# Performance work log

Hardware: AMD Instinct MI355X
Metric: run time of the kernel (lower is better)

## Reference

```python
import jax, jax.numpy as jnp
import numpy as np
import math

B, L, D, P, H, WIN, MAXLEN = 2, 2048, 256, 32, 4, 5, 16384


def setup_inputs() -> dict:
    key = jax.random.key(0)
    ks = iter(jax.random.split(key, 40))
    def w(shape, scale=0.05):
        return jax.random.normal(next(ks), shape, jnp.float32) * scale
    inp = {
        'x': jax.random.normal(next(ks), (B, L, D), jnp.float32),
        'pos_phases': jax.random.normal(next(ks), (MAXLEN, P), jnp.float32) * math.pi,
        # mem1_content_encoder
        'w_content': w((D, D)), 'b_content': jnp.zeros((D,), jnp.float32),
        # head_offset_predictors (stacked over H): Linear(D+P, D//2) -> GELU -> Linear(D//2, P+1)
        'hop_w1': w((H, D // 2, D + P)), 'hop_b1': jnp.zeros((H, D // 2), jnp.float32),
        'hop_w2': w((H, P + 1, D // 2)), 'hop_b2': jnp.zeros((H, P + 1), jnp.float32),
        # content_phase_encoder
        'w_cpe': w((P, D)), 'b_cpe': jnp.zeros((P,), jnp.float32),
        # value_encoder
        'w_val': w((D, D)), 'b_val': jnp.zeros((D,), jnp.float32),
        # kv_context_encoder
        'w_ctx': w((D, D)), 'b_ctx': jnp.zeros((D,), jnp.float32),
        # kv_storage_key: Linear(2D, D) -> GELU -> Linear(D, P)
        'kv_w1': w((D, 2 * D)), 'kv_b1': jnp.zeros((D,), jnp.float32),
        'kv_w2': w((P, D)), 'kv_b2': jnp.zeros((P,), jnp.float32),
        # store_gate: Linear(D, D//2) -> GELU -> Linear(D//2, 1) -> Sigmoid
        'sg_w1': w((D // 2, D)), 'sg_b1': jnp.zeros((D // 2,), jnp.float32),
        'sg_w2': w((1, D // 2)), 'sg_b2': jnp.zeros((1,), jnp.float32),
        # to_out: LayerNorm(D) -> Linear(D, D)
        'ln_g': jnp.ones((D,), jnp.float32), 'ln_b': jnp.zeros((D,), jnp.float32),
        'w_out': w((D, D)), 'b_out': jnp.zeros((D,), jnp.float32),
    }
    return inp


def reference(x, pos_phases, w_content, b_content, hop_w1, hop_b1, hop_w2, hop_b2,
              w_cpe, b_cpe, w_val, b_val, w_ctx, b_ctx, kv_w1, kv_b1, kv_w2, kv_b2,
              sg_w1, sg_b1, sg_w2, sg_b2, ln_g, ln_b, w_out, b_out):
    gelu = lambda t: jax.nn.gelu(t, approximate=False)  # torch exact GELU
    pp = pos_phases[:L]                      # (L,P)
    pos_cos, pos_sin = jnp.cos(pp), jnp.sin(pp)

    # ---- phasor memory 1: position-bound content cumsum ----
    content = x @ w_content.T + b_content    # (B,L,D)
    mem1_cos = jnp.cumsum(pos_cos[None, :, :, None] * content[:, :, None, :], axis=1)  # (B,L,P,D)
    mem1_sin = jnp.cumsum(pos_sin[None, :, :, None] * content[:, :, None, :], axis=1)

    # ---- per-head learned offsets ----
    offset_input = jnp.concatenate([x, jnp.broadcast_to(pp[None], (B, L, P))], axis=-1)  # (B,L,D+P)
    h1 = gelu(jnp.einsum('blf,hgf->bhlg', offset_input, hop_w1) + hop_b1[None, :, None, :])
    off = jnp.einsum('bhlg,hpg->bhlp', h1, hop_w2) + hop_b2[None, :, None, :]  # (B,H,L,P+1)
    center = jnp.tanh(off[..., :P]) * math.pi    # (B,H,L,P)
    ww = jax.nn.sigmoid(off[..., P:]) * 2 + 0.1  # (B,H,L,1)

    head_ret = jnp.zeros((B, H, L, D), x.dtype)
    tot_w = jnp.zeros((B, H, L, 1), x.dtype)
    half = WIN // 2
    for delta in range(-half, half + 1):
        wgt = jnp.exp(-0.5 * delta ** 2 / (ww ** 2 + 1e-6))
        op = center + delta * 0.1
        oc, os = jnp.cos(op), jnp.sin(op)
        qc = pos_cos[None, None] * oc - pos_sin[None, None] * os
        qs = pos_sin[None, None] * oc + pos_cos[None, None] * os
        ret = (jnp.einsum('blpd,bhlp->bhld', mem1_cos, qc)
               + jnp.einsum('blpd,bhlp->bhld', mem1_sin, qs)) / math.sqrt(P)
        head_ret = head_ret + wgt * ret
        tot_w = tot_w + wgt
    multi_head_out = (head_ret / (tot_w + 1e-6)).mean(axis=1)  # (B,L,D)

    # ---- kv phasor memory ----
    key_ph = jnp.tanh(x @ w_cpe.T + b_cpe) * math.pi            # (B,L,P)
    values = x @ w_val.T + b_val                                 # (B,L,D)
    store_gate = jax.nn.sigmoid(gelu(x @ sg_w1.T + sg_b1) @ sg_w2.T + sg_b2)  # (B,L,1)
    ctx = x @ w_ctx.T + b_ctx
    ctx_avg = jnp.cumsum(ctx, axis=1) / jnp.arange(1, L + 1, dtype=x.dtype)[None, :, None]
    storage_in = jnp.concatenate([x, ctx_avg], axis=-1)          # (B,L,2D)
    sp = jnp.tanh(gelu(storage_in @ kv_w1.T + kv_b1) @ kv_w2.T + kv_b2) * math.pi  # (B,L,P)
    gated_v = values * store_gate                                # (B,L,D)
    kv_cos = jnp.cumsum(jnp.cos(sp)[..., None] * gated_v[:, :, None, :], axis=1)  # (B,L,P,D)
    kv_sin = jnp.cumsum(jnp.sin(sp)[..., None] * gated_v[:, :, None, :], axis=1)
    gate_cum = jnp.clip(jnp.cumsum(store_gate, axis=1), 1.0, None)  # (B,L,1)
    kv_ret = (jnp.einsum('blpd,blp->bld', kv_cos, jnp.cos(key_ph))
              + jnp.einsum('blpd,blp->bld', kv_sin, jnp.sin(key_ph)))
    kv_ret = kv_ret / (jnp.sqrt(gate_cum) * math.sqrt(P))

    # ---- output projection ----
    combined = multi_head_out + kv_ret
    mu = combined.mean(-1, keepdims=True)
    var = combined.var(-1, keepdims=True)
    ln = (combined - mu) / jnp.sqrt(var + 1e-5) * ln_g + ln_b
    return x + ln @ w_out.T + b_out
```

## Files before the change

kernel.cpp:

```cpp
#include <hip/hip_runtime.h>
#include <hip/hip_bf16.h>

#define BB 2
#define LL 2048
#define DD 256
#define PP 32
#define PX 64
#define NROW (BB*LL)
#define COLS 1440
#define KIN 288
#define CC 64
#define NC (LL/CC)
#define PI_F 3.14159265358979323846f

typedef __attribute__((ext_vector_type(8))) short bf16x8;
typedef __attribute__((ext_vector_type(4))) float f32x4;

__device__ __forceinline__ float gelu_f(float v){
    return 0.5f*v*(1.0f+erff(v*0.70710678118654752440f));
}
__device__ __forceinline__ float sigm_f(float v){
    return 1.0f/(1.0f+expf(-v));
}
__device__ __forceinline__ short f2b(float v){
    __hip_bfloat16 h = __float2bfloat16(v);
    return *reinterpret_cast<short*>(&h);
}
__device__ __forceinline__ float b2f(unsigned short u){
    unsigned int x = ((unsigned int)u)<<16;
    return __uint_as_float(x);
}

__global__ void kprep(const float* w_content,const float* w_val,const float* w_ctx,
                      const float* w_cpe,const float* sg_w1,const float* hop_w1,
                      const float* b_content,const float* b_val,const float* b_ctx,
                      const float* b_cpe,const float* sg_b1,const float* hop_b1,
                      const float* pos_phases,const float* kv_w1,const float* kv_w2,
                      const float* hop_w2,const float* x,
                      short* W_catb,float* bias_cat,float* w2mem,
                      short* kvw1b,short* kvw2b,float* hop_w2T,
                      short* Xb,short* Xin2b){
    int idx = blockIdx.x*256 + threadIdx.x;
    int n1 = COLS*KIN;
    if (idx < n1){
        int row = idx / KIN, k = idx % KIN;
        float v = 0.f;
        if      (row < 256){ if (k<256) v = w_content[row*256+k]; }
        else if (row < 512){ if (k<256) v = w_val[(row-256)*256+k]; }
        else if (row < 768){ if (k<256) v = w_ctx[(row-512)*256+k]; }
        else if (row < 800){ if (k<256) v = w_cpe[(row-768)*256+k]; }
        else if (row < 928){ if (k<256) v = sg_w1[(row-800)*256+k]; }
        else               { v = hop_w1[(row-928)*288 + k]; }
        W_catb[idx] = f2b(v);
        return;
    }
    idx -= n1;
    if (idx < COLS){
        int row = idx; float v = 0.f;
        if      (row < 256) v = b_content[row];
        else if (row < 512) v = b_val[row-256];
        else if (row < 768) v = b_ctx[row-512];
        else if (row < 800) v = b_cpe[row-768];
        else if (row < 928) v = sg_b1[row-800];
        else                v = hop_b1[row-928];
        bias_cat[row] = v;
        return;
    }
    idx -= COLS;
    if (idx < LL*PP){
        int l = idx/PP, p = idx%PP;
        float ph = pos_phases[l*PP+p];
        w2mem[l*PX+p]     = cosf(ph);
        w2mem[l*PX+32+p]  = sinf(ph);
        return;
    }
    idx -= LL*PP;
    if (idx < 256*512){ kvw1b[idx] = f2b(kv_w1[idx]); return; }
    idx -= 256*512;
    if (idx < 32*256){ kvw2b[idx] = f2b(kv_w2[idx]); return; }
    idx -= 32*256;
    if (idx < 128*132){
        int k=idx/132, o=idx%132;
        hop_w2T[idx] = hop_w2[o*128+k];
        return;
    }
    idx -= 128*132;
    if (idx < NROW*KIN){
        int r = idx / KIN, d = idx % KIN;
        float v;
        if (d < 256){ v = x[(size_t)r*DD + d]; Xin2b[(size_t)r*512 + d] = f2b(v); }
        else          v = pos_phases[(r % LL)*PP + (d-256)];
        Xb[idx] = f2b(v);
    }
}

__global__ __launch_bounds__(256) void kA_gemm(const short* Xb,const short* Wb,short* Yb){
    int t=threadIdx.x;
    int wid=t>>6, l=t&63;
    int q=blockIdx.x;
    int ct=q%15, rt=q/15;
    int r0=rt*64 + wid*16;
    int c0=ct*96;
    int lr=l&15, lk=(l>>4)*8;
    const short* ap = Xb + (size_t)(r0+lr)*KIN + lk;
    const short* bp = Wb + (size_t)(c0+lr)*KIN + lk;
    f32x4 acc[6];
    #pragma unroll
    for (int f=0;f<6;f++) acc[f]=(f32x4){0.f,0.f,0.f,0.f};
    for (int ks=0;ks<9;ks++){
        bf16x8 a = *(const bf16x8*)(ap + ks*32);
        #pragma unroll
        for (int f=0;f<6;f++){
            bf16x8 b = *(const bf16x8*)(bp + (size_t)f*16*KIN + ks*32);
            acc[f] = __builtin_amdgcn_mfma_f32_16x16x32_bf16(a,b,acc[f],0,0,0);
        }
    }
    int orow = r0 + (l>>4)*4;
    int ocol = c0 + lr;
    #pragma unroll
    for (int f=0;f<6;f++){
        #pragma unroll
        for (int qq=0;qq<4;qq++){
            Yb[(size_t)(orow+qq)*COLS + ocol + 16*f] = f2b(acc[f][qq]);
        }
    }
}

__global__ __launch_bounds__(256,4) void kA_post(const short* Yb,const float* bias_cat,
        const float* sg_w2,const float* sg_b2,
        const float* hop_w2T,const float* hop_b2,const float* pos_phases,
        short* contentb,short* gatedvb,float* ctx,float* key_ph,
        float* store_gate,float* coef_mem){
    __shared__ float yb[4][1448];
    __shared__ float red[4][32];
    __shared__ float offb[4][136];
    __shared__ float scl[4][4];
    __shared__ float sgvv[4];
    int t=threadIdx.x;
    int r0=blockIdx.x*4;
    {
        const ushort4* Yu4 = (const ushort4*)(Yb) + (size_t)r0*360;
        #pragma unroll
        for (int i=0;i<6;i++){
            int chunk=i*256+t;
            if (chunk<1440){
                int r=chunk/360, c=(chunk%360)*4;
                ushort4 s4 = Yu4[chunk];
                float4 bc = *(const float4*)&bias_cat[c];
                yb[r][c+0]=b2f(s4.x)+bc.x;
                yb[r][c+1]=b2f(s4.y)+bc.y;
                yb[r][c+2]=b2f(s4.z)+bc.z;
                yb[r][c+3]=b2f(s4.w)+bc.w;
            }
        }
    }
    __syncthreads();
    #pragma unroll
    for (int r=0;r<4;r++){
        contentb[(size_t)(r0+r)*DD+t] = f2b(yb[r][t]);
        ctx[(size_t)(r0+r)*DD+t]      = yb[r][512+t];
    }
    #pragma unroll
    for (int j=0;j<8;j++){
        int idx=j*256+t, r=idx>>9, g=idx&511;
        yb[r][928+g] = gelu_f(yb[r][928+g]);
    }
    if (t<128){
        int r=t>>5, j=t&31;
        float s=0.f;
        #pragma unroll
        for (int k=0;k<4;k++){
            int jj=j+32*k;
            s += gelu_f(yb[r][800+jj])*sg_w2[jj];
        }
        red[r][j]=s;
        key_ph[(size_t)(r0+r)*PP+j] = tanhf(yb[r][768+j])*PI_F;
    }
    __syncthreads();
    if (t<128){
        int r=t>>5;
        float s=red[r][t&31];
        #pragma unroll
        for (int off=16;off>=1;off>>=1) s += __shfl_down(s,off,32);
        if ((t&31)==0){
            float g=sigm_f(s+sg_b2[0]);
            sgvv[r]=g;
            store_gate[r0+r]=g;
        }
    }
    for (int sIdx=t; sIdx<528; sIdx+=256){
        int r=sIdx/132, o=sIdx%132, h=o/33;
        const float* yh=&yb[r][928+h*128];
        float a0=0.f,a1=0.f,a2=0.f,a3=0.f;
        #pragma unroll 8
        for (int k=0;k<128;k+=4){
            a0 += hop_w2T[(size_t)(k+0)*132+o]*yh[k+0];
            a1 += hop_w2T[(size_t)(k+1)*132+o]*yh[k+1];
            a2 += hop_w2T[(size_t)(k+2)*132+o]*yh[k+2];
            a3 += hop_w2T[(size_t)(k+3)*132+o]*yh[k+3];
        }
        offb[r][o]=a0+a1+a2+a3+hop_b2[o];
    }
    __syncthreads();
    #pragma unroll
    for (int r=0;r<4;r++) gatedvb[(size_t)(r0+r)*DD+t]=f2b(yb[r][256+t]*sgvv[r]);
    if (t<16){
        int r=t>>2, h=t&3;
        const float c01=0.99500416527802576610f;
        const float c02=0.98006657784124163112f;
        float ww=sigm_f(offb[r][h*33+32])*2.0f+0.1f;
        float iw=1.0f/(ww*ww+1e-6f);
        float w1=expf(-0.5f*iw);
        float w2=expf(-2.0f*iw);
        float tot=1.0f+2.0f*w1+2.0f*w2;
        float Wc =1.0f+2.0f*w1*c01+2.0f*w2*c02;
        scl[r][h]=Wc/((tot+1e-6f)*5.65685424949238019520f*4.0f);
    }
    __syncthreads();
    if (t<128){
        int r=t>>5, p=t&31;
        int l=(r0+r)%LL;
        float ppv=pos_phases[l*PP+p];
        float ca=0.f, sb=0.f;
        #pragma unroll
        for (int h=0;h<4;h++){
            float center=tanhf(offb[r][h*33+p])*PI_F;
            float ang=ppv+center;
            float sc=scl[r][h];
            ca+=sc*cosf(ang);
            sb+=sc*sinf(ang);
        }
        coef_mem[(size_t)(r0+r)*PX+p]=ca;
        coef_mem[(size_t)(r0+r)*PX+32+p]=sb;
    }
}

__global__ void k3a_ctxsum(const float* ctx,float* ctxcs){
    int t=threadIdx.x;
    int bi=blockIdx.x;
    int c=bi%NC, b=bi/NC;
    float s=0.f;
    for (int i=0;i<CC;i++) s += ctx[((size_t)b*LL + c*CC + i)*DD + t];
    ctxcs[(size_t)(b*NC+c)*DD + t] = s;
}
__global__ void k3c_ctxavg(const float* ctx,const float* ctxcs,short* Xin2b){
    int t=threadIdx.x;
    int bi=blockIdx.x;
    int c=bi%NC, b=bi/NC;
    float run=0.f;
    for (int cc=0;cc<c;cc++) run += ctxcs[(size_t)(b*NC+cc)*DD+t];
    for (int i=0;i<CC;i++){
        int l = c*CC+i;
        run += ctx[((size_t)b*LL+l)*DD + t];
        Xin2b[((size_t)b*LL+l)*512 + 256 + t] = f2b(run/(float)(l+1));
    }
}

__global__ __launch_bounds__(256) void kgate(const float* store_gate,const float* key_ph,
                                             float* coefkv){
    __shared__ float sh[2048];
    __shared__ float red[256];
    __shared__ float rsgS[64];
    int t=threadIdx.x, q=blockIdx.x;
    int c=q&31, b=q>>5;
    int n=(c+1)*CC;
    for (int i=t;i<n;i+=256) sh[i]=store_gate[(size_t)b*LL+i];
    __syncthreads();
    float p=0.f;
    for (int i=t;i<c*CC;i+=256) p+=sh[i];
    red[t]=p;
    __syncthreads();
    for (int off=128;off>=1;off>>=1){
        if (t<off) red[t]+=red[t+off];
        __syncthreads();
    }
    float S0=red[0];
    if (t<64){
        float s=sh[c*CC+t];
        #pragma unroll
        for (int off=1;off<64;off<<=1){
            float v=__shfl_up(s,off);
            if (t>=off) s+=v;
        }
        rsgS[t]=rsqrtf(fmaxf(S0+s,1.0f)*32.0f);
    }
    __syncthreads();
    #pragma unroll
    for (int j=0;j<8;j++){
        int g2=t+j*256;
        int l=g2>>5, pp=g2&31;
        float a=key_ph[((size_t)b*LL + c*CC + l)*PP + pp];
        float rv=rsgS[l];
        coefkv[((size_t)b*LL + c*CC + l)*PX + pp]      = cosf(a)*rv;
        coefkv[((size_t)b*LL + c*CC + l)*PX + 32 + pp] = sinf(a)*rv;
    }
}

__global__ __launch_bounds__(256) void k3d1(const short* Xin2b,const short* kvw1b,
        const float* kv_b1, short* Hb){
    int t=threadIdx.x;
    int wid=t>>6, l=t&63;
    int q=blockIdx.x;
    int nt=q&3, mt=q>>2;
    int r0=mt*64 + wid*16;
    int c0=nt*64;
    int lr=l&15, lk=(l>>4)*8;
    const short* ap = Xin2b + (size_t)(r0+lr)*512 + lk;
    const short* bp = kvw1b + (size_t)(c0+lr)*512 + lk;
    f32x4 acc[4];
    #pragma unroll
    for (int f=0;f<4;f++) acc[f]=(f32x4){0.f,0.f,0.f,0.f};
    for (int ks=0;ks<16;ks++){
        bf16x8 a = *(const bf16x8*)(ap + ks*32);
        #pragma unroll
        for (int f=0;f<4;f++){
            bf16x8 b = *(const bf16x8*)(bp + (size_t)f*16*512 + ks*32);
            acc[f] = __builtin_amdgcn_mfma_f32_16x16x32_bf16(a,b,acc[f],0,0,0);
        }
    }
    int orow = r0 + (l>>4)*4;
    #pragma unroll
    for (int f=0;f<4;f++){
        int oc = c0 + lr + 16*f;
        float bias = kv_b1[oc];
        #pragma unroll
        for (int qq=0;qq<4;qq++){
            Hb[(size_t)(orow+qq)*256 + oc] = f2b(gelu_f(acc[f][qq]+bias));
        }
    }
}

__global__ __launch_bounds__(256) void k3d2(const short* Hb,const short* kvw2b,
        const float* kv_b2, float* w2kv){
    int t=threadIdx.x;
    int wid=t>>6, l=t&63;
    int mt=blockIdx.x;
    int r0=mt*64 + wid*16;
    int lr=l&15, lk=(l>>4)*8;
    const short* ap = Hb + (size_t)(r0+lr)*256 + lk;
    const short* bp = kvw2b + (size_t)lr*256 + lk;
    f32x4 acc0=(f32x4){0.f,0.f,0.f,0.f};
    f32x4 acc1=(f32x4){0.f,0.f,0.f,0.f};
    for (int ks=0;ks<8;ks++){
        bf16x8 a  = *(const bf16x8*)(ap + ks*32);
        bf16x8 b0 = *(const bf16x8*)(bp + ks*32);
        bf16x8 b1 = *(const bf16x8*)(bp + (size_t)16*256 + ks*32);
        acc0 = __builtin_amdgcn_mfma_f32_16x16x32_bf16(a,b0,acc0,0,0,0);
        acc1 = __builtin_amdgcn_mfma_f32_16x16x32_bf16(a,b1,acc1,0,0,0);
    }
    int orow=r0+(l>>4)*4;
    #pragma unroll
    for (int f=0;f<2;f++){
        int p = lr + 16*f;
        float bias = kv_b2[p];
        f32x4 av = f? acc1:acc0;
        #pragma unroll
        for (int qq=0;qq<4;qq++){
            float sp=tanhf(av[qq]+bias)*PI_F;
            w2kv[(size_t)(orow+qq)*PX + p]    = cosf(sp);
            w2kv[(size_t)(orow+qq)*PX + 32+p] = sinf(sp);
        }
    }
}

__global__ __launch_bounds__(256) void k4_chunksum(
        const short* valA,const float* w2A,int w2bA,
        const short* valB,const float* w2B,int w2bB,
        float* CS){
    __shared__ float w2s[CC][PX];
    int t=threadIdx.x, q=blockIdx.x;
    int dq=q&3, c=(q>>2)&31, b=(q>>7)&1, inst=q>>8;
    const short* val = inst? valB:valA;
    const float* w2  = inst? w2B:w2A;
    int w2b          = inst? w2bB:w2bA;
    for (int i=0;i<16;i++){
        int idx=i*256+t;
        int l=idx>>6, p=idx&63;
        w2s[l][p]=w2[(size_t)w2b*b + (size_t)(c*CC+l)*PX + p];
    }
    __syncthreads();
    int d=t&63, pg=t>>6;
    float acc[16];
    #pragma unroll
    for (int j=0;j<16;j++) acc[j]=0.f;
    const short* vp = val + ((size_t)b*LL + c*CC)*DD + dq*64 + d;
    for (int l=0;l<CC;l++){
        float v = b2f((unsigned short)vp[(size_t)l*DD]);
        const float4* wr=(const float4*)&w2s[l][pg*16];
        #pragma unroll
        for (int k=0;k<4;k++){
            float4 w=wr[k];
            acc[4*k]   += w.x*v;
            acc[4*k+1] += w.y*v;
            acc[4*k+2] += w.z*v;
            acc[4*k+3] += w.w*v;
        }
    }
    float* cp = CS + (((size_t)(inst*BB+b)*NC + c)*PX + pg*16)*DD + dq*64 + d;
    #pragma unroll
    for (int j=0;j<16;j++) cp[(size_t)j*DD]=acc[j];
}

__global__ void k5_prefix(float* CS){
    int g=blockIdx.x*256+threadIdx.x;
    int d=g&255, p2=(g>>8)&63, b=(g>>14)&1, inst=g>>15;
    float run=0.f;
    for (int c=0;c<NC;c++){
        size_t idx=(((size_t)(inst*BB+b)*NC+c)*PX+p2)*DD+d;
        float tmp=CS[idx]; CS[idx]=run; run+=tmp;
    }
}

__global__ __launch_bounds__(256) void k6_attn(
        const float* coefA,const float* w2A,int w2bA,const short* valA,float* outA,
        const float* coefB,const float* w2B,int w2bB,const short* valB,float* outB,
        const float* CS){
    __shared__ float coefs[16][PX];
    __shared__ float w2s[CC][PX];
    __shared__ float S[16][CC];
    int t=threadIdx.x, q=blockIdx.x;
    int rq=q&3, qc=(q>>2)&31, b=(q>>7)&1, inst=q>>8;
    const float* coef = inst? coefB:coefA;
    const float* w2   = inst? w2B:w2A;
    int w2b           = inst? w2bB:w2bA;
    const short* val  = inst? valB:valA;
    float* out        = inst? outB:outA;
    int gr0 = rq*16;
    #pragma unroll
    for (int i=0;i<4;i++){
        int idx=i*256+t;
        int r=idx>>6, p=idx&63;
        coefs[r][p]=coef[((size_t)b*LL + qc*CC + gr0 + r)*PX + p];
    }
    for (int i=0;i<16;i++){
        int idx=i*256+t;
        int l=idx>>6, p=idx&63;
        w2s[l][p]=w2[(size_t)w2b*b + (size_t)(qc*CC+l)*PX + p];
    }
    __syncthreads();
    {
        int lp=t&63, rr=t>>6;
        #pragma unroll
        for (int rj=0;rj<4;rj++){
            int r=rr*4+rj;
            int gr=gr0+r;
            float s=0.f;
            if (lp<=gr){
                const float4* cr=(const float4*)&coefs[r][0];
                const float4* wr=(const float4*)&w2s[lp][0];
                #pragma unroll
                for (int k=0;k<16;k++){
                    float4 cv=cr[k], wv=wr[k];
                    s += cv.x*wv.x+cv.y*wv.y+cv.z*wv.z+cv.w*wv.w;
                }
            }
            S[r][lp]=s;
        }
    }
    __syncthreads();
    {
        float acc[16];
        #pragma unroll
        for (int i=0;i<16;i++) acc[i]=0.f;
        const float* pfx = CS + (((size_t)(inst*BB+b)*NC + qc)*PX)*DD + t;
        for (int p=0;p<PX;p++){
            float pf = pfx[(size_t)p*DD];
            #pragma unroll
            for (int i=0;i<16;i++) acc[i] += coefs[i][p]*pf;
        }
        const short* vptr = val + ((size_t)b*LL + qc*CC)*DD + t;
        int kmax = gr0+16;
        for (int lp=0; lp<kmax; lp++){
            float v = b2f((unsigned short)vptr[(size_t)lp*DD]);
            #pragma unroll
            for (int i=0;i<16;i++) acc[i] += S[i][lp]*v;
        }
        float* op = out + ((size_t)b*LL + qc*CC + gr0)*DD + t;
        #pragma unroll
        for (int i=0;i<16;i++) op[(size_t)i*DD] = acc[i];
    }
}

__global__ __launch_bounds__(256) void k7_final(const float* comb,const float* kvout,
        const float* x,const float* ln_g,const float* ln_b,const float* w_out,const float* b_out,
        float* out){
    __shared__ float cb[8][DD];
    __shared__ float red[8][64];
    __shared__ float mvm[8][2];
    int t=threadIdx.x, r0=blockIdx.x*8;
    for (int r=0;r<8;r++){
        float v = comb[(size_t)(r0+r)*DD + t] + kvout[(size_t)(r0+r)*DD + t];
        cb[r][t]=v;
    }
    __syncthreads();
    {
        int rr=t>>5, ii=t&31;
        float s=0.f, s2=0.f;
        #pragma unroll
        for (int j=0;j<8;j++){
            float v=cb[rr][ii*8+j];
            s+=v; s2+=v*v;
        }
        red[rr][ii]=s; red[rr][32+ii]=s2;
    }
    __syncthreads();
    if (t<8){
        float s=0.f,s2=0.f;
        for (int i=0;i<32;i++){ s+=red[t][i]; s2+=red[t][32+i]; }
        float mu=s/256.f;
        float var=s2/256.f - mu*mu;
        mvm[t][0]=mu; mvm[t][1]=rsqrtf(var+1e-5f);
    }
    __syncthreads();
    for (int r=0;r<8;r++){
        float v=(cb[r][t]-mvm[r][0])*mvm[r][1]*ln_g[t]+ln_b[t];
        cb[r][t]=v;
    }
    __syncthreads();
    {
        int c=t;
        const float4* wp=(const float4*)(w_out + (size_t)c*DD);
        float acc[8];
        #pragma unroll
        for (int r=0;r<8;r++) acc[r]=0.f;
        for (int k4=0;k4<64;k4++){
            float4 w=wp[k4];
            #pragma unroll
            for (int r=0;r<8;r++){
                float4 lv=*(const float4*)&cb[r][k4*4];
                acc[r]+=w.x*lv.x+w.y*lv.y+w.z*lv.z+w.w*lv.w;
            }
        }
        #pragma unroll
        for (int r=0;r<8;r++){
            float o = x[(size_t)(r0+r)*DD + c] + acc[r] + b_out[c];
            out[(size_t)(r0+r)*DD + c] = o;
        }
    }
}

extern "C" void kernel_launch(void* const* d_in, const int* in_sizes, int n_in,
                              void* d_out, int out_size, void* d_ws, size_t ws_size,
                              hipStream_t stream){
    (void)in_sizes; (void)n_in; (void)out_size; (void)ws_size;
    const float* x         =(const float*)d_in[0];
    const float* pos_phases=(const float*)d_in[1];
    const float* w_content =(const float*)d_in[2];
    const float* b_content =(const float*)d_in[3];
    const float* hop_w1    =(const float*)d_in[4];
    const float* hop_b1    =(const float*)d_in[5];
    const float* hop_w2    =(const float*)d_in[6];
    const float* hop_b2    =(const float*)d_in[7];
    const float* w_cpe     =(const float*)d_in[8];
    const float* b_cpe     =(const float*)d_in[9];
    const float* w_val     =(const float*)d_in[10];
    const float* b_val     =(const float*)d_in[11];
    const float* w_ctx     =(const float*)d_in[12];
    const float* b_ctx     =(const float*)d_in[13];
    const float* kv_w1     =(const float*)d_in[14];
    const float* kv_b1     =(const float*)d_in[15];
    const float* kv_w2     =(const float*)d_in[16];
    const float* kv_b2     =(const float*)d_in[17];
    const float* sg_w1     =(const float*)d_in[18];
    const float* sg_b1     =(const float*)d_in[19];
    const float* sg_w2     =(const float*)d_in[20];
    const float* sg_b2     =(const float*)d_in[21];
    const float* ln_g      =(const float*)d_in[22];
    const float* ln_b      =(const float*)d_in[23];
    const float* w_out     =(const float*)d_in[24];
    const float* b_out     =(const float*)d_in[25];

    float* ws=(float*)d_ws;
    size_t o=0;
    short* W_catb  =(short*)(ws+o); o+=(size_t)COLS*KIN/2;
    short* Xb      =(short*)(ws+o); o+=(size_t)NROW*KIN/2;
    short* kvw1b   =(short*)(ws+o); o+=(size_t)256*512/2;
    short* kvw2b   =(short*)(ws+o); o+=(size_t)32*256/2;
    short* Hb      =(short*)(ws+o); o+=(size_t)NROW*256/2;
    short* contentb=(short*)(ws+o); o+=(size_t)NROW*DD/2;
    short* gatedvb =(short*)(ws+o); o+=(size_t)NROW*DD/2;
    float* bias_cat=ws+o; o+=COLS;
    float* hop_w2T =ws+o; o+=(size_t)128*132;
    float* w2mem   =ws+o; o+=(size_t)LL*PX;
    float* ctx     =ws+o; o+=(size_t)NROW*DD;
    float* xin2_kv =ws+o; o+=(size_t)NROW*DD;
    float* key_ph  =ws+o; o+=(size_t)NROW*PP;
    float* store_gate=ws+o; o+=NROW;
    float* coef_mem=ws+o; o+=(size_t)NROW*PX;
    float* coefkv  =ws+o; o+=(size_t)NROW*PX;
    float* w2kv    =ws+o; o+=(size_t)NROW*PX;
    float* ctxcs   =ws+o; o+=(size_t)BB*NC*DD;
    float* CS      =ws+o; o+=(size_t)2*BB*NC*PX*DD;
    short* Yb      =(short*)CS;
    short* Xin2b   =(short*)xin2_kv;
    float* comb  = ctx;
    float* kvout = xin2_kv;

    int prep_total = COLS*KIN + COLS + LL*PP + 256*512 + 32*256 + 128*132 + NROW*KIN;
    kprep<<<(prep_total+255)/256,256,0,stream>>>(
                                 w_content,w_val,w_ctx,w_cpe,sg_w1,hop_w1,
                                 b_content,b_val,b_ctx,b_cpe,sg_b1,hop_b1,
                                 pos_phases,kv_w1,kv_w2,hop_w2,x,
                                 W_catb,bias_cat,w2mem,kvw1b,kvw2b,hop_w2T,Xb,Xin2b);
    kA_gemm<<<960,256,0,stream>>>(Xb,W_catb,Yb);
    kA_post<<<NROW/4,256,0,stream>>>(Yb,bias_cat,sg_w2,sg_b2,hop_w2T,hop_b2,pos_phases,
                                     contentb,gatedvb,ctx,key_ph,store_gate,coef_mem);
    k3a_ctxsum<<<BB*NC,256,0,stream>>>(ctx,ctxcs);
    k3c_ctxavg<<<BB*NC,256,0,stream>>>(ctx,ctxcs,Xin2b);
    kgate<<<BB*NC,256,0,stream>>>(store_gate,key_ph,coefkv);
    k3d1<<<256,256,0,stream>>>(Xin2b,kvw1b,kv_b1,Hb);
    k3d2<<<64,256,0,stream>>>(Hb,kvw2b,kv_b2,w2kv);
    k4_chunksum<<<2*BB*NC*4,256,0,stream>>>(contentb,w2mem,0,
                                            gatedvb,w2kv,LL*PX,CS);
    k5_prefix<<<2*BB*PX*DD/256,256,0,stream>>>(CS);
    k6_attn<<<2*BB*NC*4,256,0,stream>>>(coef_mem,w2mem,0,contentb,comb,
                                        coefkv,w2kv,LL*PX,gatedvb,kvout,CS);
    k7_final<<<NROW/8,256,0,stream>>>(comb,kvout,x,ln_g,ln_b,w_out,b_out,
                                      (float*)d_out);
}
```

Measured before the change: 168.2 us.

## Use MFMA for output projection, merge gate and kv GEMM kernels, restructure attention

The final LayerNorm+output projection now runs on bf16 MFMA with a bf16 copy of w_out made in the prep kernel, and each block handles 16 rows instead of 8. The kgate and k3d1 kernels are merged into one launch that splits work by block index. k5_prefix loads all chunk values into registers before the scan. k6_attn is reorganized so each block computes the full 64x64 intra-chunk score matrix for a 64-column slice of D, with padded shared memory. Together these aim to cut scalar FP32 FLOPs and launch overhead, at the cost of bf16 rounding in the output GEMM and redundant score computation across the four D-slices.

```diff
diff --git a/kernel.cpp b/kernel.cpp
--- a/kernel.cpp
+++ b/kernel.cpp
@@ -36,9 +36,9 @@
                       const float* b_content,const float* b_val,const float* b_ctx,
                       const float* b_cpe,const float* sg_b1,const float* hop_b1,
                       const float* pos_phases,const float* kv_w1,const float* kv_w2,
-                      const float* hop_w2,const float* x,
+                      const float* hop_w2,const float* w_out,const float* x,
                       short* W_catb,float* bias_cat,float* w2mem,
-                      short* kvw1b,short* kvw2b,float* hop_w2T,
+                      short* kvw1b,short* kvw2b,float* hop_w2T,short* w_outb,
                       short* Xb,short* Xin2b){
     int idx = blockIdx.x*256 + threadIdx.x;
     int n1 = COLS*KIN;
@@ -85,6 +85,8 @@
         return;
     }
     idx -= 128*132;
+    if (idx < 256*256){ w_outb[idx] = f2b(w_out[idx]); return; }
+    idx -= 256*256;
     if (idx < NROW*KIN){
         int r = idx / KIN, d = idx % KIN;
         float v;
@@ -256,12 +258,46 @@
     }
 }
 
-__global__ __launch_bounds__(256) void kgate(const float* store_gate,const float* key_ph,
-                                             float* coefkv){
+__global__ __launch_bounds__(256) void kmid(const short* Xin2b,const short* kvw1b,
+        const float* kv_b1, short* Hb,
+        const float* store_gate,const float* key_ph,float* coefkv){
     __shared__ float sh[2048];
     __shared__ float red[256];
     __shared__ float rsgS[64];
-    int t=threadIdx.x, q=blockIdx.x;
+    int t=threadIdx.x;
+    if (blockIdx.x < 256){
+        int wid=t>>6, l=t&63;
+        int q=blockIdx.x;
+        int nt=q&3, mt=q>>2;
+        int r0=mt*64 + wid*16;
+        int c0=nt*64;
+        int lr=l&15, lk=(l>>4)*8;
+        const short* ap = Xin2b + (size_t)(r0+lr)*512 + lk;
+        const short* bp = kvw1b + (size_t)(c0+lr)*512 + lk;
+        f32x4 acc[4];
+        #pragma unroll
+        for (int f=0;f<4;f++) acc[f]=(f32x4){0.f,0.f,0.f,0.f};
+        for (int ks=0;ks<16;ks++){
+            bf16x8 a = *(const bf16x8*)(ap + ks*32);
+            #pragma unroll
+            for (int f=0;f<4;f++){
+                bf16x8 b = *(const bf16x8*)(bp + (size_t)f*16*512 + ks*32);
+                acc[f] = __builtin_amdgcn_mfma_f32_16x16x32_bf16(a,b,acc[f],0,0,0);
+            }
+        }
+        int orow = r0 + (l>>4)*4;
+        #pragma unroll
+        for (int f=0;f<4;f++){
+            int oc = c0 + lr + 16*f;
+            float bias = kv_b1[oc];
+            #pragma unroll
+            for (int qq=0;qq<4;qq++){
+                Hb[(size_t)(orow+qq)*256 + oc] = f2b(gelu_f(acc[f][qq]+bias));
+            }
+        }
+        return;
+    }
+    int q=blockIdx.x-256;
     int c=q&31, b=q>>5;
     int n=(c+1)*CC;
     for (int i=t;i<n;i+=256) sh[i]=store_gate[(size_t)b*LL+i];
@@ -293,40 +329,6 @@
         float rv=rsgS[l];
         coefkv[((size_t)b*LL + c*CC + l)*PX + pp]      = cosf(a)*rv;
         coefkv[((size_t)b*LL + c*CC + l)*PX + 32 + pp] = sinf(a)*rv;
-    }
-}
-
-__global__ __launch_bounds__(256) void k3d1(const short* Xin2b,const short* kvw1b,
-        const float* kv_b1, short* Hb){
-    int t=threadIdx.x;
-    int wid=t>>6, l=t&63;
-    int q=blockIdx.x;
-    int nt=q&3, mt=q>>2;
-    int r0=mt*64 + wid*16;
-    int c0=nt*64;
-    int lr=l&15, lk=(l>>4)*8;
-    const short* ap = Xin2b + (size_t)(r0+lr)*512 + lk;
-    const short* bp = kvw1b + (size_t)(c0+lr)*512 + lk;
-    f32x4 acc[4];
-    #pragma unroll
-    for (int f=0;f<4;f++) acc[f]=(f32x4){0.f,0.f,0.f,0.f};
-    for (int ks=0;ks<16;ks++){
-        bf16x8 a = *(const bf16x8*)(ap + ks*32);
-        #pragma unroll
-        for (int f=0;f<4;f++){
-            bf16x8 b = *(const bf16x8*)(bp + (size_t)f*16*512 + ks*32);
-            acc[f] = __builtin_amdgcn_mfma_f32_16x16x32_bf16(a,b,acc[f],0,0,0);
-        }
-    }
-    int orow = r0 + (l>>4)*4;
-    #pragma unroll
-    for (int f=0;f<4;f++){
-        int oc = c0 + lr + 16*f;
-        float bias = kv_b1[oc];
-        #pragma unroll
-        for (int qq=0;qq<4;qq++){
-            Hb[(size_t)(orow+qq)*256 + oc] = f2b(gelu_f(acc[f][qq]+bias));
-        }
     }
 }
 
@@ -404,10 +406,16 @@
 __global__ void k5_prefix(float* CS){
     int g=blockIdx.x*256+threadIdx.x;
     int d=g&255, p2=(g>>8)&63, b=(g>>14)&1, inst=g>>15;
+    size_t base=(((size_t)(inst*BB+b)*NC)*PX+p2)*DD+d;
+    float v[NC];
+    #pragma unroll
+    for (int c=0;c<NC;c++) v[c]=CS[base+(size_t)c*PX*DD];
     float run=0.f;
+    #pragma unroll
     for (int c=0;c<NC;c++){
-        size_t idx=(((size_t)(inst*BB+b)*NC+c)*PX+p2)*DD+d;
-        float tmp=CS[idx]; CS[idx]=run; run+=tmp;
+        float tmp=v[c];
+        CS[base+(size_t)c*PX*DD]=run;
+        run+=tmp;
     }
 }
 
@@ -415,126 +423,131 @@
         const float* coefA,const float* w2A,int w2bA,const short* valA,float* outA,
         const float* coefB,const float* w2B,int w2bB,const short* valB,float* outB,
         const float* CS){
-    __shared__ float coefs[16][PX];
+    __shared__ float coefs[CC][PX+1];
     __shared__ float w2s[CC][PX];
-    __shared__ float S[16][CC];
+    __shared__ float S[CC][CC+1];
     int t=threadIdx.x, q=blockIdx.x;
-    int rq=q&3, qc=(q>>2)&31, b=(q>>7)&1, inst=q>>8;
+    int dq=q&3, qc=(q>>2)&31, b=(q>>7)&1, inst=q>>8;
     const float* coef = inst? coefB:coefA;
     const float* w2   = inst? w2B:w2A;
     int w2b           = inst? w2bB:w2bA;
     const short* val  = inst? valB:valA;
     float* out        = inst? outB:outA;
-    int gr0 = rq*16;
-    #pragma unroll
-    for (int i=0;i<4;i++){
-        int idx=i*256+t;
-        int r=idx>>6, p=idx&63;
-        coefs[r][p]=coef[((size_t)b*LL + qc*CC + gr0 + r)*PX + p];
-    }
+    int d0 = dq*64;
     for (int i=0;i<16;i++){
         int idx=i*256+t;
         int l=idx>>6, p=idx&63;
-        w2s[l][p]=w2[(size_t)w2b*b + (size_t)(qc*CC+l)*PX + p];
+        coefs[l][p]=coef[((size_t)b*LL + qc*CC + l)*PX + p];
+        w2s[l][p]  =w2[(size_t)w2b*b + (size_t)(qc*CC+l)*PX + p];
     }
     __syncthreads();
     {
-        int lp=t&63, rr=t>>6;
-        #pragma unroll
-        for (int rj=0;rj<4;rj++){
-            int r=rr*4+rj;
-            int gr=gr0+r;
+        int l=t&63, lpb=(t>>6)*16;
+        float cf[PX];
+        #pragma unroll
+        for (int p=0;p<PX;p++) cf[p]=coefs[l][p];
+        for (int qq=0;qq<16;qq++){
+            int lp=lpb+qq;
             float s=0.f;
-            if (lp<=gr){
-                const float4* cr=(const float4*)&coefs[r][0];
+            if (lp<=l){
                 const float4* wr=(const float4*)&w2s[lp][0];
                 #pragma unroll
                 for (int k=0;k<16;k++){
-                    float4 cv=cr[k], wv=wr[k];
-                    s += cv.x*wv.x+cv.y*wv.y+cv.z*wv.z+cv.w*wv.w;
+                    float4 w=wr[k];
+                    s += w.x*cf[4*k]+w.y*cf[4*k+1]+w.z*cf[4*k+2]+w.w*cf[4*k+3];
                 }
             }
-            S[r][lp]=s;
+            S[l][lp]=s;
         }
     }
     __syncthreads();
     {
+        int d=t&63, lq=t>>6;
         float acc[16];
         #pragma unroll
         for (int i=0;i<16;i++) acc[i]=0.f;
-        const float* pfx = CS + (((size_t)(inst*BB+b)*NC + qc)*PX)*DD + t;
+        const float* pfx = CS + (((size_t)(inst*BB+b)*NC + qc)*PX)*DD + d0 + d;
         for (int p=0;p<PX;p++){
             float pf = pfx[(size_t)p*DD];
             #pragma unroll
-            for (int i=0;i<16;i++) acc[i] += coefs[i][p]*pf;
-        }
-        const short* vptr = val + ((size_t)b*LL + qc*CC)*DD + t;
-        int kmax = gr0+16;
+            for (int i=0;i<16;i++) acc[i] += coefs[lq*16+i][p]*pf;
+        }
+        const short* vptr = val + ((size_t)b*LL + qc*CC)*DD + d0 + d;
+        int kmax = lq*16+16;
         for (int lp=0; lp<kmax; lp++){
             float v = b2f((unsigned short)vptr[(size_t)lp*DD]);
             #pragma unroll
-            for (int i=0;i<16;i++) acc[i] += S[i][lp]*v;
-        }
-        float* op = out + ((size_t)b*LL + qc*CC + gr0)*DD + t;
+            for (int i=0;i<16;i++) acc[i] += S[lq*16+i][lp]*v;
+        }
+        float* op = out + ((size_t)b*LL + qc*CC + lq*16)*DD + d0 + d;
         #pragma unroll
         for (int i=0;i<16;i++) op[(size_t)i*DD] = acc[i];
     }
 }
 
 __global__ __launch_bounds__(256) void k7_final(const float* comb,const float* kvout,
-        const float* x,const float* ln_g,const float* ln_b,const float* w_out,const float* b_out,
+        const float* x,const float* ln_g,const float* ln_b,const short* w_outb,const float* b_out,
         float* out){
-    __shared__ float cb[8][DD];
-    __shared__ float red[8][64];
-    __shared__ float mvm[8][2];
-    int t=threadIdx.x, r0=blockIdx.x*8;
-    for (int r=0;r<8;r++){
-        float v = comb[(size_t)(r0+r)*DD + t] + kvout[(size_t)(r0+r)*DD + t];
-        cb[r][t]=v;
+    __shared__ float cb[16][260];
+    __shared__ short Ab[16][264];
+    __shared__ float red[16][32];
+    __shared__ float mvm[16][2];
+    int t=threadIdx.x, r0=blockIdx.x*16;
+    #pragma unroll
+    for (int i=0;i<16;i++){
+        int idx=i*256+t;
+        int r=idx>>8, c=idx&255;
+        cb[r][c]=comb[(size_t)(r0+r)*DD+c]+kvout[(size_t)(r0+r)*DD+c];
     }
     __syncthreads();
     {
-        int rr=t>>5, ii=t&31;
-        float s=0.f, s2=0.f;
-        #pragma unroll
-        for (int j=0;j<8;j++){
-            float v=cb[rr][ii*8+j];
+        int r=t>>4, j=t&15;
+        float s=0.f,s2=0.f;
+        #pragma unroll
+        for (int k=0;k<16;k++){
+            float v=cb[r][j+16*k];
             s+=v; s2+=v*v;
         }
-        red[rr][ii]=s; red[rr][32+ii]=s2;
-    }
-    __syncthreads();
-    if (t<8){
+        red[r][j]=s; red[r][16+j]=s2;
+    }
+    __syncthreads();
+    if (t<16){
         float s=0.f,s2=0.f;
-        for (int i=0;i<32;i++){ s+=red[t][i]; s2+=red[t][32+i]; }
+        #pragma unroll
+        for (int j=0;j<16;j++){ s+=red[t][j]; s2+=red[t][16+j]; }
         float mu=s/256.f;
-        float var=s2/256.f - mu*mu;
+        float var=s2/256.f-mu*mu;
         mvm[t][0]=mu; mvm[t][1]=rsqrtf(var+1e-5f);
     }
     __syncthreads();
-    for (int r=0;r<8;r++){
-        float v=(cb[r][t]-mvm[r][0])*mvm[r][1]*ln_g[t]+ln_b[t];
-        cb[r][t]=v;
-    }
-    __syncthreads();
-    {
-        int c=t;
-        const float4* wp=(const float4*)(w_out + (size_t)c*DD);
-        float acc[8];
-        #pragma unroll
-        for (int r=0;r<8;r++) acc[r]=0.f;
-        for (int k4=0;k4<64;k4++){
-            float4 w=wp[k4];
-            #pragma unroll
-            for (int r=0;r<8;r++){
-                float4 lv=*(const float4*)&cb[r][k4*4];
-                acc[r]+=w.x*lv.x+w.y*lv.y+w.z*lv.z+w.w*lv.w;
-            }
-        }
-        #pragma unroll
-        for (int r=0;r<8;r++){
-            float o = x[(size_t)(r0+r)*DD + c] + acc[r] + b_out[c];
-            out[(size_t)(r0+r)*DD + c] = o;
+    #pragma unroll
+    for (int i=0;i<16;i++){
+        int idx=i*256+t;
+        int r=idx>>8, c=idx&255;
+        Ab[r][c]=f2b((cb[r][c]-mvm[r][0])*mvm[r][1]*ln_g[c]+ln_b[c]);
+    }
+    __syncthreads();
+    int wid=t>>6, l=t&63;
+    int lr=l&15, lk=(l>>4)*8;
+    f32x4 acc[4];
+    #pragma unroll
+    for (int f=0;f<4;f++) acc[f]=(f32x4){0.f,0.f,0.f,0.f};
+    for (int ks=0;ks<8;ks++){
+        bf16x8 a = *(const bf16x8*)&Ab[lr][lk+ks*32];
+        #pragma unroll
+        for (int f=0;f<4;f++){
+            bf16x8 bv = *(const bf16x8*)(w_outb + (size_t)(wid*64+f*16+lr)*256 + lk + ks*32);
+            acc[f] = __builtin_amdgcn_mfma_f32_16x16x32_bf16(a,bv,acc[f],0,0,0);
+        }
+    }
+    int orow = r0 + (l>>4)*4;
+    #pragma unroll
+    for (int f=0;f<4;f++){
+        int oc = wid*64 + f*16 + lr;
+        float bo = b_out[oc];
+        #pragma unroll
+        for (int qq=0;qq<4;qq++){
+            out[(size_t)(orow+qq)*DD + oc] = x[(size_t)(orow+qq)*DD + oc] + acc[f][qq] + bo;
         }
     }
 }
@@ -576,6 +589,7 @@
     short* Xb      =(short*)(ws+o); o+=(size_t)NROW*KIN/2;
     short* kvw1b   =(short*)(ws+o); o+=(size_t)256*512/2;
     short* kvw2b   =(short*)(ws+o); o+=(size_t)32*256/2;
+    short* w_outb  =(short*)(ws+o); o+=(size_t)256*256/2;
     short* Hb      =(short*)(ws+o); o+=(size_t)NROW*256/2;
     short* contentb=(short*)(ws+o); o+=(size_t)NROW*DD/2;
     short* gatedvb =(short*)(ws+o); o+=(size_t)NROW*DD/2;
@@ -596,25 +610,24 @@
     float* comb  = ctx;
     float* kvout = xin2_kv;
 
-    int prep_total = COLS*KIN + COLS + LL*PP + 256*512 + 32*256 + 128*132 + NROW*KIN;
+    int prep_total = COLS*KIN + COLS + LL*PP + 256*512 + 32*256 + 128*132 + 256*256 + NROW*KIN;
     kprep<<<(prep_total+255)/256,256,0,stream>>>(
                                  w_content,w_val,w_ctx,w_cpe,sg_w1,hop_w1,
                                  b_content,b_val,b_ctx,b_cpe,sg_b1,hop_b1,
-                                 pos_phases,kv_w1,kv_w2,hop_w2,x,
-                                 W_catb,bias_cat,w2mem,kvw1b,kvw2b,hop_w2T,Xb,Xin2b);
+                                 pos_phases,kv_w1,kv_w2,hop_w2,w_out,x,
+                                 W_catb,bias_cat,w2mem,kvw1b,kvw2b,hop_w2T,w_outb,Xb,Xin2b);
     kA_gemm<<<960,256,0,stream>>>(Xb,W_catb,Yb);
     kA_post<<<NROW/4,256,0,stream>>>(Yb,bias_cat,sg_w2,sg_b2,hop_w2T,hop_b2,pos_phases,
                                      contentb,gatedvb,ctx,key_ph,store_gate,coef_mem);
     k3a_ctxsum<<<BB*NC,256,0,stream>>>(ctx,ctxcs);
     k3c_ctxavg<<<BB*NC,256,0,stream>>>(ctx,ctxcs,Xin2b);
-    kgate<<<BB*NC,256,0,stream>>>(store_gate,key_ph,coefkv);
-    k3d1<<<256,256,0,stream>>>(Xin2b,kvw1b,kv_b1,Hb);
+    kmid<<<256+BB*NC,256,0,stream>>>(Xin2b,kvw1b,kv_b1,Hb,store_gate,key_ph,coefkv);
     k3d2<<<64,256,0,stream>>>(Hb,kvw2b,kv_b2,w2kv);
     k4_chunksum<<<2*BB*NC*4,256,0,stream>>>(contentb,w2mem,0,
                                             gatedvb,w2kv,LL*PX,CS);
     k5_prefix<<<2*BB*PX*DD/256,256,0,stream>>>(CS);
     k6_attn<<<2*BB*NC*4,256,0,stream>>>(coef_mem,w2mem,0,contentb,comb,
                                         coefkv,w2kv,LL*PX,gatedvb,kvout,CS);
-    k7_final<<<NROW/8,256,0,stream>>>(comb,kvout,x,ln_g,ln_b,w_out,b_out,
-                                      (float*)d_out);
-}
+    k7_final<<<NROW/16,256,0,stream>>>(comb,kvout,x,ln_g,ln_b,w_outb,b_out,
+                                       (float*)d_out);
+}
```

After: 147.7 us. -12.2%, faster.
